# Performance work log

Measured on AMD Instinct MI355X. Metric: run time of the kernel, lower is better.

Reference implementation:

```python
import jax, jax.numpy as jnp
import numpy as np


def setup_inputs() -> dict:
    key = jax.random.key(0)
    embeddings = jax.random.normal(key, (4, 2048, 128), dtype=jnp.float32)
    return {"embeddings": embeddings}


def _pairwise_dist(x):
    # x: [N, D] -> Euclidean distance matrix [N, N] (matches torch.cdist, p=2)
    sq = jnp.sum(x * x, axis=-1)  # [N]
    d2 = sq[:, None] + sq[None, :] - 2.0 * (x @ x.T)
    d2 = jnp.maximum(d2, 0.0)
    # safe sqrt: exact 0 on the diagonal / coincident points, no NaN grads
    safe = jnp.where(d2 > 0.0, d2, 1.0)
    return jnp.where(d2 > 0.0, jnp.sqrt(safe), 0.0)


def reference(embeddings) -> jnp.ndarray:
    b, s, d = embeddings.shape
    x = embeddings.reshape(b * s, d)
    dist = _pairwise_dist(x)                 # [N, N]
    mean_dist = jnp.mean(dist)
    # torch.std default: unbiased (ddof=1) over all elements
    std_dist = jnp.std(dist, ddof=1)
    return std_dist / (mean_dist + 1e-08)
```

## Files before the change

kernel.cpp:

```cpp
#include <hip/hip_runtime.h>
#include <hip/hip_bf16.h>
#include <math.h>


#define NPTS   8192
#define DIM    128
#define BT     256
#define NT2    (NPTS / BT)
#define NBLK   (NT2 * (NT2 + 1) / 2)
#define NPREP  (NPTS / 32)
#define NTILES (NPTS / 128)
#define NTOTSQ (NTILES * NTILES)

typedef __attribute__((ext_vector_type(8))) short short8;
typedef __attribute__((ext_vector_type(4))) float f32x4;

typedef const __attribute__((address_space(1))) void* gas_ptr;
typedef __attribute__((address_space(3))) void* las_ptr;

__device__ __forceinline__ void gload16(const void* g, void* l) {
    __builtin_amdgcn_global_load_lds((gas_ptr)g, (las_ptr)l, 16, 0, 0);
}
__device__ __forceinline__ float fsqrt(float x) {
    return __builtin_amdgcn_sqrtf(x);
}

#define VMCNT(n) asm volatile("s_waitcnt vmcnt(" #n ")" ::: "memory")
#define RBAR()   __builtin_amdgcn_s_barrier()

__global__ __launch_bounds__(256)
void ph_prep(const float* __restrict__ x, ushort* __restrict__ xb,
             float* __restrict__ sq, float* __restrict__ cs_part)
{
    __shared__ float xs[32][129];
    const int tid = threadIdx.x;
    const int rw  = tid >> 3;
    const int row = blockIdx.x * 32 + rw;
    const int seg = tid & 7;
    const float4* p = reinterpret_cast<const float4*>(x + (size_t)row * DIM + seg * 16);
    float v[16];
    {
        float4 a = p[0], b = p[1], c = p[2], d = p[3];
        v[0]=a.x; v[1]=a.y; v[2]=a.z; v[3]=a.w;  v[4]=b.x; v[5]=b.y; v[6]=b.z; v[7]=b.w;
        v[8]=c.x; v[9]=c.y; v[10]=c.z; v[11]=c.w; v[12]=d.x; v[13]=d.y; v[14]=d.z; v[15]=d.w;
    }
    float s = 0.f;
    ushort h[16];
#pragma unroll
    for (int j = 0; j < 16; ++j) {
        __hip_bfloat16 hb = __float2bfloat16(v[j]);
        h[j] = *reinterpret_cast<ushort*>(&hb);
        s = fmaf(v[j], v[j], s);
        xs[rw][seg * 16 + j] = v[j];
    }
    short8 o0, o1;
#pragma unroll
    for (int j = 0; j < 8; ++j) { o0[j] = (short)h[j]; o1[j] = (short)h[j+8]; }
    short8* dst = reinterpret_cast<short8*>(xb + (size_t)row * DIM + seg * 16);
    dst[0] = o0; dst[1] = o1;
    s += __shfl_xor(s, 1); s += __shfl_xor(s, 2); s += __shfl_xor(s, 4);
    if (seg == 0) sq[row] = s;
    __syncthreads();
    if (tid < DIM) {
        float c = 0.f;
#pragma unroll 8
        for (int r = 0; r < 32; ++r) c += xs[r][tid];
        cs_part[blockIdx.x * DIM + tid] = c;
    }
}

__global__ __launch_bounds__(512)
void ph_gram(const ushort* __restrict__ xb, const float* __restrict__ sq,
             double* __restrict__ partials)
{
    const int f   = blockIdx.x;
    const int tid = threadIdx.x;

    int bi = (int)((65.0f - fsqrt((float)(4225 - 8 * f))) * 0.5f);
    while ((bi + 1) * 32 - ((bi + 1) * bi) / 2 <= f) ++bi;
    while (bi * 32 - (bi * (bi - 1)) / 2 > f) --bi;
    const int bj = bi + (f - (bi * 32 - (bi * (bi - 1)) / 2));

    __shared__ ushort Aq[4][BT * 32];
    __shared__ ushort Bq[4][BT * 32];
    __shared__ double rr[8];

    const int lane = tid & 63;
    const int wv   = tid >> 6;
    const int wr2  = wv >> 2;
    const int wc4  = wv & 3;

    const char* gA = (const char*)(xb + (size_t)bi * BT * DIM);
    const char* gB = (const char*)(xb + (size_t)bj * BT * DIM);

    const bool  stA  = wv < 4;
    const char* gsrc = stA ? gA : gB;
    const int   c0   = (wv & 3) * 4;
    const int   lrow = lane >> 2;
    const int   lks  = (lane & 3) * 16;

#define STAGE(q)                                                              \
    {                                                                         \
        char* dst_ = stA ? (char*)Aq[q] : (char*)Bq[q];                       \
        _Pragma("unroll")                                                     \
        for (int c = 0; c < 4; ++c) {                                         \
            const int chunk = c0 + c;                                         \
            const int row   = chunk * 16 + lrow;                              \
            const size_t go = (size_t)row * 256 + (q) * 64 + lks;             \
            gload16(gsrc + go, dst_ + chunk * 1024);                          \
        }                                                                     \
    }

    f32x4 acc[8][4];
#pragma unroll
    for (int m = 0; m < 8; ++m)
#pragma unroll
        for (int n = 0; n < 4; ++n) acc[m][n] = (f32x4){0.f, 0.f, 0.f, 0.f};

#define COMPUTE(q)                                                            \
    {                                                                         \
        const int kb = (lane >> 4) * 16;                                      \
        short8 af[8], bfr[4];                                                 \
        _Pragma("unroll")                                                     \
        for (int m = 0; m < 8; ++m) {                                         \
            const int row = wr2 * 128 + m * 16 + (lane & 15);                 \
            af[m] = *reinterpret_cast<const short8*>(                         \
                (const char*)Aq[q] + row * 64 + kb);                          \
        }                                                                     \
        _Pragma("unroll")                                                     \
        for (int n = 0; n < 4; ++n) {                                         \
            const int col = wc4 * 64 + n * 16 + (lane & 15);                  \
            bfr[n] = *reinterpret_cast<const short8*>(                        \
                (const char*)Bq[q] + col * 64 + kb);                          \
        }                                                                     \
        __builtin_amdgcn_s_setprio(1);                                        \
        _Pragma("unroll")                                                     \
        for (int m = 0; m < 8; ++m)                                           \
            _Pragma("unroll")                                                 \
            for (int n = 0; n < 4; ++n)                                       \
                acc[m][n] = __builtin_amdgcn_mfma_f32_16x16x32_bf16(          \
                    af[m], bfr[n], acc[m][n], 0, 0, 0);                       \
        __builtin_amdgcn_s_setprio(0);                                        \
    }

    STAGE(0);
    STAGE(1);
    VMCNT(4); RBAR();
    COMPUTE(0);
    STAGE(2);
    VMCNT(4); RBAR();
    COMPUTE(1);
    STAGE(3);

    const float* sqA = sq + bi * BT + wr2 * 128 + (lane >> 4) * 4;
    const float* sqB = sq + bj * BT + wc4 * 64 + (lane & 15);
    float4 na[4];
    float  nb[4];
#pragma unroll
    for (int m = 0; m < 4; ++m) na[m] = *reinterpret_cast<const float4*>(sqA + m * 32);
#pragma unroll
    for (int n = 0; n < 4; ++n) nb[n] = sqB[n * 16];

    VMCNT(12); RBAR();
    COMPUTE(2);
    VMCNT(8); RBAR();
    COMPUTE(3);
    VMCNT(0);

    float s1a = 0.f, s1b = 0.f, s1c = 0.f, s1d = 0.f;
    const bool diag = (bi == bj);
    if (!diag) {
#pragma unroll
        for (int m = 0; m < 4; ++m) {
            const float4 v = na[m];
#pragma unroll
            for (int n = 0; n < 4; ++n) {
                s1a += fsqrt(fmaxf(fmaf(-2.f, acc[2*m][n][0], v.x + nb[n]), 0.f));
                s1b += fsqrt(fmaxf(fmaf(-2.f, acc[2*m][n][1], v.y + nb[n]), 0.f));
                s1c += fsqrt(fmaxf(fmaf(-2.f, acc[2*m][n][2], v.z + nb[n]), 0.f));
                s1d += fsqrt(fmaxf(fmaf(-2.f, acc[2*m][n][3], v.w + nb[n]), 0.f));
            }
        }
    }
    if (!diag) {
#pragma unroll
        for (int m = 1; m < 8; m += 2) {
            const float4 v = *reinterpret_cast<const float4*>(sqA + m * 16);
#pragma unroll
            for (int n = 0; n < 4; ++n) {
                s1a += fsqrt(fmaxf(fmaf(-2.f, acc[m][n][0], v.x + nb[n]), 0.f));
                s1b += fsqrt(fmaxf(fmaf(-2.f, acc[m][n][1], v.y + nb[n]), 0.f));
                s1c += fsqrt(fmaxf(fmaf(-2.f, acc[m][n][2], v.z + nb[n]), 0.f));
                s1d += fsqrt(fmaxf(fmaf(-2.f, acc[m][n][3], v.w + nb[n]), 0.f));
            }
        }
    } else {
#pragma unroll
        for (int m = 0; m < 8; ++m) {
            const float4 v = *reinterpret_cast<const float4*>(sqA + m * 16);
            const float nav[4] = {v.x, v.y, v.z, v.w};
#pragma unroll
            for (int n = 0; n < 4; ++n) {
                const int col = wc4 * 64 + n * 16 + (lane & 15);
#pragma unroll
                for (int r = 0; r < 4; ++r) {
                    const int row = wr2 * 128 + m * 16 + (lane >> 4) * 4 + r;
                    float d = fmaxf(fmaf(-2.f, acc[m][n][r], nav[r] + nb[n]), 0.f);
                    if (row == col) d = 0.f;
                    s1a += fsqrt(d);
                }
            }
        }
    }
    float s1 = (s1a + s1b) + (s1c + s1d);
#pragma unroll
    for (int off = 1; off < 64; off <<= 1) s1 += __shfl_xor(s1, off);
    const double w = diag ? 1.0 : 2.0;
    if (lane == 0) rr[wv] = (double)s1 * w;
    __syncthreads();
    if (tid == 0) {
        double t1 = 0.0;
#pragma unroll
        for (int i = 0; i < 8; ++i) t1 += rr[i];
        partials[f] = t1;
    }
#undef STAGE
#undef COMPUTE
}

__global__ __launch_bounds__(256)
void ph_finalize(const double* __restrict__ partials, const float* __restrict__ sq,
                 const float* __restrict__ cs_part, float* __restrict__ out)
{
    __shared__ double r1[256], r2[256], r3[128];
    const int tid = threadIdx.x;
    double s1 = 0.0;
    for (int i = tid; i < NBLK; i += 256) s1 += partials[i];
    double sn = 0.0;
    for (int k = 0; k < NPTS / 256; ++k) sn += (double)sq[tid + k * 256];
    r1[tid] = s1; r2[tid] = sn;
    if (tid < DIM) {
        double c = 0.0;
        for (int b = 0; b < NPREP; ++b) c += (double)cs_part[b * DIM + tid];
        r3[tid] = c * c;
    }
    __syncthreads();
    for (int off = 128; off > 0; off >>= 1) {
        if (tid < off) {
            r1[tid] += r1[tid + off];
            r2[tid] += r2[tid + off];
            if (off >= 2 && tid < (off >> 1) && off <= 128) {}
        }
        __syncthreads();
    }
    for (int off = 64; off > 0; off >>= 1) {
        if (tid < off) r3[tid] += r3[tid + off];
        __syncthreads();
    }
    if (tid == 0) {
        const double M    = (double)NPTS * (double)NPTS;
        const double S1   = r1[0];
        const double S2   = 2.0 * (double)NPTS * r2[0] - 2.0 * r3[0];
        const double mean = S1 / M;
        double var = (S2 - S1 * S1 / M) / (M - 1.0);
        if (var < 0.0) var = 0.0;
        out[0] = (float)(sqrt(var) / (mean + 1e-8));
    }
}

#define LSTR 132
__global__ __launch_bounds__(256)
void ph_pair_kernel(const float* __restrict__ x, double* __restrict__ partials)
{
    const int bi  = blockIdx.y;
    const int bj  = blockIdx.x;
    const int tid = threadIdx.x;
    const int flat = bi * NTILES + bj;
    if (bj < bi) {
        if (tid == 0) { partials[2*flat] = 0.0; partials[2*flat+1] = 0.0; }
        return;
    }
    __shared__ __align__(16) float As[128 * LSTR];
    __shared__ __align__(16) float Bs[128 * LSTR];
    __shared__ float  nA[128];
    __shared__ float  nB[128];
    __shared__ double red1[256];
    __shared__ double red2[256];
    const float* Ab = x + (size_t)bi * 128 * DIM;
    const float* Bb = x + (size_t)bj * 128 * DIM;
#pragma unroll
    for (int it = 0; it < 16; ++it) {
        const int e   = (tid + it * 256) * 4;
        const int row = e >> 7;
        const int k   = e & 127;
        float4 va = *reinterpret_cast<const float4*>(Ab + e);
        As[(k+0)*LSTR + row] = va.x; As[(k+1)*LSTR + row] = va.y;
        As[(k+2)*LSTR + row] = va.z; As[(k+3)*LSTR + row] = va.w;
        float4 vb = *reinterpret_cast<const float4*>(Bb + e);
        Bs[(k+0)*LSTR + row] = vb.x; Bs[(k+1)*LSTR + row] = vb.y;
        Bs[(k+2)*LSTR + row] = vb.z; Bs[(k+3)*LSTR + row] = vb.w;
    }
    __syncthreads();
    if (tid < 128) {
        float s = 0.f;
#pragma unroll 8
        for (int k = 0; k < DIM; ++k) { float v = As[k*LSTR + tid]; s = fmaf(v, v, s); }
        nA[tid] = s;
    } else {
        const int r = tid - 128;
        float s = 0.f;
#pragma unroll 8
        for (int k = 0; k < DIM; ++k) { float v = Bs[k*LSTR + r]; s = fmaf(v, v, s); }
        nB[r] = s;
    }
    __syncthreads();
    const int tx = tid & 15, ty = tid >> 4;
    const int ra = ty * 8, cb = tx * 8;
    float acc[8][8];
#pragma unroll
    for (int r = 0; r < 8; ++r)
#pragma unroll
        for (int c = 0; c < 8; ++c) acc[r][c] = 0.f;
#pragma unroll 4
    for (int k = 0; k < DIM; ++k) {
        const float4 a0 = *reinterpret_cast<const float4*>(&As[k*LSTR + ra]);
        const float4 a1 = *reinterpret_cast<const float4*>(&As[k*LSTR + ra + 4]);
        const float4 b0 = *reinterpret_cast<const float4*>(&Bs[k*LSTR + cb]);
        const float4 b1 = *reinterpret_cast<const float4*>(&Bs[k*LSTR + cb + 4]);
        const float a[8] = {a0.x,a0.y,a0.z,a0.w,a1.x,a1.y,a1.z,a1.w};
        const float b[8] = {b0.x,b0.y,b0.z,b0.w,b1.x,b1.y,b1.z,b1.w};
#pragma unroll
        for (int r = 0; r < 8; ++r)
#pragma unroll
            for (int c = 0; c < 8; ++c)
                acc[r][c] = fmaf(a[r], b[c], acc[r][c]);
    }
    double s1 = 0.0, s2 = 0.0;
    const int gi0 = bi*128 + ra, gj0 = bj*128 + cb;
#pragma unroll
    for (int r = 0; r < 8; ++r) {
#pragma unroll
        for (int c = 0; c < 8; ++c) {
            float d2 = nA[ra+r] + nB[cb+c] - 2.0f * acc[r][c];
            d2 = fmaxf(d2, 0.0f);
            if (gi0 + r == gj0 + c) d2 = 0.0f;
            s1 += (double)sqrtf(d2);
            s2 += (double)d2;
        }
    }
    const double w = (bi == bj) ? 1.0 : 2.0;
    s1 *= w; s2 *= w;
    red1[tid] = s1; red2[tid] = s2;
    __syncthreads();
    for (int off = 128; off > 0; off >>= 1) {
        if (tid < off) { red1[tid] += red1[tid+off]; red2[tid] += red2[tid+off]; }
        __syncthreads();
    }
    if (tid == 0) { partials[2*flat] = red1[0]; partials[2*flat+1] = red2[0]; }
}

__global__ __launch_bounds__(256)
void ph_finalize_sq(const double* __restrict__ partials, float* __restrict__ out)
{
    __shared__ double r1[256], r2[256];
    const int tid = threadIdx.x;
    double s1 = 0.0, s2 = 0.0;
    for (int i = tid; i < NTOTSQ; i += 256) { s1 += partials[2*i]; s2 += partials[2*i+1]; }
    r1[tid] = s1; r2[tid] = s2;
    __syncthreads();
    for (int off = 128; off > 0; off >>= 1) {
        if (tid < off) { r1[tid] += r1[tid+off]; r2[tid] += r2[tid+off]; }
        __syncthreads();
    }
    if (tid == 0) {
        const double M    = (double)NPTS * (double)NPTS;
        const double mean = r1[0] / M;
        double var = (r2[0] - r1[0]*r1[0]/M) / (M - 1.0);
        if (var < 0.0) var = 0.0;
        out[0] = (float)(sqrt(var) / (mean + 1e-8));
    }
}

extern "C" void kernel_launch(void* const* d_in, const int* in_sizes, int n_in,
                              void* d_out, int out_size, void* d_ws, size_t ws_size,
                              hipStream_t stream)
{
    const float* x = (const float*)d_in[0];
    float* out     = (float*)d_out;

    const size_t XB_OFF = 0;
    const size_t SQ_OFF = (size_t)NPTS * DIM * sizeof(ushort);
    const size_t CS_OFF = SQ_OFF + NPTS * sizeof(float);
    const size_t PT_OFF = CS_OFF + (size_t)NPREP * DIM * sizeof(float);
    const size_t NEEDED = PT_OFF + (size_t)NBLK * sizeof(double);

    if (ws_size >= NEEDED) {
        ushort* xb       = (ushort*)((char*)d_ws + XB_OFF);
        float*  sq       = (float*) ((char*)d_ws + SQ_OFF);
        float*  cs_part  = (float*) ((char*)d_ws + CS_OFF);
        double* partials = (double*)((char*)d_ws + PT_OFF);

        ph_prep<<<NPREP, 256, 0, stream>>>(x, xb, sq, cs_part);
        ph_gram<<<NBLK, 512, 0, stream>>>(xb, sq, partials);
        ph_finalize<<<1, 256, 0, stream>>>(partials, sq, cs_part, out);
    } else {
        double* partials = (double*)d_ws;
        ph_pair_kernel<<<dim3(NTILES, NTILES), 256, 0, stream>>>(x, partials);
        ph_finalize_sq<<<1, 256, 0, stream>>>(partials, out);
    }
}
```

Before: 39.72 us.

## Split gram tile across 16 waves with XOR-swizzled LDS and two-stage K

The gram kernel now runs 1024 threads (16 waves), so each wave owns a 64x64 sub-tile instead of 128x64. K is staged in two halves of 64 into double LDS buffers with an XOR swizzle, replacing four 32-wide stages. The hand-placed vmcnt/barrier pipeline gives way to plain __syncthreads. The aim is more waves to hide latency, fewer LDS bank conflicts on fragment reads, and lower per-wave register pressure, at the cost of a shallower load/compute overlap.

```diff
diff --git a/kernel.cpp b/kernel.cpp
--- a/kernel.cpp
+++ b/kernel.cpp
@@ -24,9 +24,6 @@
 __device__ __forceinline__ float fsqrt(float x) {
     return __builtin_amdgcn_sqrtf(x);
 }
-
-#define VMCNT(n) asm volatile("s_waitcnt vmcnt(" #n ")" ::: "memory")
-#define RBAR()   __builtin_amdgcn_s_barrier()
 
 __global__ __launch_bounds__(256)
 void ph_prep(const float* __restrict__ x, ushort* __restrict__ xb,
@@ -69,7 +66,7 @@
     }
 }
 
-__global__ __launch_bounds__(512)
+__global__ __launch_bounds__(1024, 4)
 void ph_gram(const ushort* __restrict__ xb, const float* __restrict__ sq,
              double* __restrict__ partials)
 {
@@ -81,110 +78,90 @@
     while (bi * 32 - (bi * (bi - 1)) / 2 > f) --bi;
     const int bj = bi + (f - (bi * 32 - (bi * (bi - 1)) / 2));
 
-    __shared__ ushort Aq[4][BT * 32];
-    __shared__ ushort Bq[4][BT * 32];
-    __shared__ double rr[8];
+    __shared__ ushort A0[BT * 64], B0[BT * 64];
+    __shared__ ushort A1[BT * 64], B1[BT * 64];
+    __shared__ double rr[32];
 
     const int lane = tid & 63;
     const int wv   = tid >> 6;
-    const int wr2  = wv >> 2;
-    const int wc4  = wv & 3;
+    const int wr   = wv >> 2;
+    const int wc   = wv & 3;
 
     const char* gA = (const char*)(xb + (size_t)bi * BT * DIM);
     const char* gB = (const char*)(xb + (size_t)bj * BT * DIM);
 
-    const bool  stA  = wv < 4;
+    const bool  stA  = wv < 8;
     const char* gsrc = stA ? gA : gB;
-    const int   c0   = (wv & 3) * 4;
-    const int   lrow = lane >> 2;
-    const int   lks  = (lane & 3) * 16;
-
-#define STAGE(q)                                                              \
+    const int   c0   = (wv & 7) * 4;
+    const int   srow = lane >> 3;
+    const int   skb  = (lane & 7) * 16;
+
+#define STAGE(h, dA, dB)                                                      \
     {                                                                         \
-        char* dst_ = stA ? (char*)Aq[q] : (char*)Bq[q];                       \
+        char* dst_ = stA ? (char*)(dA) : (char*)(dB);                         \
         _Pragma("unroll")                                                     \
         for (int c = 0; c < 4; ++c) {                                         \
             const int chunk = c0 + c;                                         \
-            const int row   = chunk * 16 + lrow;                              \
-            const size_t go = (size_t)row * 256 + (q) * 64 + lks;             \
+            const int row   = chunk * 8 + srow;                               \
+            const size_t go = (size_t)row * 256 + (h) * 128                   \
+                              + (skb ^ ((row & 7) << 4));                     \
             gload16(gsrc + go, dst_ + chunk * 1024);                          \
         }                                                                     \
     }
 
-    f32x4 acc[8][4];
-#pragma unroll
-    for (int m = 0; m < 8; ++m)
+    f32x4 acc[4][4];
+#pragma unroll
+    for (int m = 0; m < 4; ++m)
 #pragma unroll
         for (int n = 0; n < 4; ++n) acc[m][n] = (f32x4){0.f, 0.f, 0.f, 0.f};
 
-#define COMPUTE(q)                                                            \
+#define COMPUTE(dA, dB)                                                       \
     {                                                                         \
-        const int kb = (lane >> 4) * 16;                                      \
-        short8 af[8], bfr[4];                                                 \
         _Pragma("unroll")                                                     \
-        for (int m = 0; m < 8; ++m) {                                         \
-            const int row = wr2 * 128 + m * 16 + (lane & 15);                 \
-            af[m] = *reinterpret_cast<const short8*>(                         \
-                (const char*)Aq[q] + row * 64 + kb);                          \
+        for (int ks = 0; ks < 2; ++ks) {                                      \
+            const int kb = ks * 64 + (lane >> 4) * 16;                        \
+            short8 af[4], bfr[4];                                             \
+            _Pragma("unroll")                                                 \
+            for (int m = 0; m < 4; ++m) {                                     \
+                const int row = wr * 64 + m * 16 + (lane & 15);               \
+                af[m] = *reinterpret_cast<const short8*>(                     \
+                    (const char*)(dA) + row * 128 + (kb ^ ((row & 7) << 4))); \
+            }                                                                 \
+            _Pragma("unroll")                                                 \
+            for (int n = 0; n < 4; ++n) {                                     \
+                const int col = wc * 64 + n * 16 + (lane & 15);               \
+                bfr[n] = *reinterpret_cast<const short8*>(                    \
+                    (const char*)(dB) + col * 128 + (kb ^ ((col & 7) << 4))); \
+            }                                                                 \
+            __builtin_amdgcn_s_setprio(1);                                    \
+            _Pragma("unroll")                                                 \
+            for (int m = 0; m < 4; ++m)                                       \
+                _Pragma("unroll")                                             \
+                for (int n = 0; n < 4; ++n)                                   \
+                    acc[m][n] = __builtin_amdgcn_mfma_f32_16x16x32_bf16(      \
+                        af[m], bfr[n], acc[m][n], 0, 0, 0);                   \
+            __builtin_amdgcn_s_setprio(0);                                    \
         }                                                                     \
-        _Pragma("unroll")                                                     \
-        for (int n = 0; n < 4; ++n) {                                         \
-            const int col = wc4 * 64 + n * 16 + (lane & 15);                  \
-            bfr[n] = *reinterpret_cast<const short8*>(                        \
-                (const char*)Bq[q] + col * 64 + kb);                          \
-        }                                                                     \
-        __builtin_amdgcn_s_setprio(1);                                        \
-        _Pragma("unroll")                                                     \
-        for (int m = 0; m < 8; ++m)                                           \
-            _Pragma("unroll")                                                 \
-            for (int n = 0; n < 4; ++n)                                       \
-                acc[m][n] = __builtin_amdgcn_mfma_f32_16x16x32_bf16(          \
-                    af[m], bfr[n], acc[m][n], 0, 0, 0);                       \
-        __builtin_amdgcn_s_setprio(0);                                        \
-    }
-
-    STAGE(0);
-    STAGE(1);
-    VMCNT(4); RBAR();
-    COMPUTE(0);
-    STAGE(2);
-    VMCNT(4); RBAR();
-    COMPUTE(1);
-    STAGE(3);
-
-    const float* sqA = sq + bi * BT + wr2 * 128 + (lane >> 4) * 4;
-    const float* sqB = sq + bj * BT + wc4 * 64 + (lane & 15);
-    float4 na[4];
-    float  nb[4];
-#pragma unroll
-    for (int m = 0; m < 4; ++m) na[m] = *reinterpret_cast<const float4*>(sqA + m * 32);
+    }
+
+    STAGE(0, A0, B0);
+    __syncthreads();
+    STAGE(1, A1, B1);
+    COMPUTE(A0, B0);
+    __syncthreads();
+    COMPUTE(A1, B1);
+
+    const float* sqA = sq + bi * BT + wr * 64 + (lane >> 4) * 4;
+    const float* sqB = sq + bj * BT + wc * 64 + (lane & 15);
+    float nb[4];
 #pragma unroll
     for (int n = 0; n < 4; ++n) nb[n] = sqB[n * 16];
-
-    VMCNT(12); RBAR();
-    COMPUTE(2);
-    VMCNT(8); RBAR();
-    COMPUTE(3);
-    VMCNT(0);
 
     float s1a = 0.f, s1b = 0.f, s1c = 0.f, s1d = 0.f;
     const bool diag = (bi == bj);
     if (!diag) {
 #pragma unroll
         for (int m = 0; m < 4; ++m) {
-            const float4 v = na[m];
-#pragma unroll
-            for (int n = 0; n < 4; ++n) {
-                s1a += fsqrt(fmaxf(fmaf(-2.f, acc[2*m][n][0], v.x + nb[n]), 0.f));
-                s1b += fsqrt(fmaxf(fmaf(-2.f, acc[2*m][n][1], v.y + nb[n]), 0.f));
-                s1c += fsqrt(fmaxf(fmaf(-2.f, acc[2*m][n][2], v.z + nb[n]), 0.f));
-                s1d += fsqrt(fmaxf(fmaf(-2.f, acc[2*m][n][3], v.w + nb[n]), 0.f));
-            }
-        }
-    }
-    if (!diag) {
-#pragma unroll
-        for (int m = 1; m < 8; m += 2) {
             const float4 v = *reinterpret_cast<const float4*>(sqA + m * 16);
 #pragma unroll
             for (int n = 0; n < 4; ++n) {
@@ -196,15 +173,15 @@
         }
     } else {
 #pragma unroll
-        for (int m = 0; m < 8; ++m) {
+        for (int m = 0; m < 4; ++m) {
             const float4 v = *reinterpret_cast<const float4*>(sqA + m * 16);
             const float nav[4] = {v.x, v.y, v.z, v.w};
 #pragma unroll
             for (int n = 0; n < 4; ++n) {
-                const int col = wc4 * 64 + n * 16 + (lane & 15);
+                const int col = wc * 64 + n * 16 + (lane & 15);
 #pragma unroll
                 for (int r = 0; r < 4; ++r) {
-                    const int row = wr2 * 128 + m * 16 + (lane >> 4) * 4 + r;
+                    const int row = wr * 64 + m * 16 + (lane >> 4) * 4 + r;
                     float d = fmaxf(fmaf(-2.f, acc[m][n][r], nav[r] + nb[n]), 0.f);
                     if (row == col) d = 0.f;
                     s1a += fsqrt(d);
@@ -221,7 +198,7 @@
     if (tid == 0) {
         double t1 = 0.0;
 #pragma unroll
-        for (int i = 0; i < 8; ++i) t1 += rr[i];
+        for (int i = 0; i < 16; ++i) t1 += rr[i];
         partials[f] = t1;
     }
 #undef STAGE
@@ -246,11 +223,7 @@
     }
     __syncthreads();
     for (int off = 128; off > 0; off >>= 1) {
-        if (tid < off) {
-            r1[tid] += r1[tid + off];
-            r2[tid] += r2[tid + off];
-            if (off >= 2 && tid < (off >> 1) && off <= 128) {}
-        }
+        if (tid < off) { r1[tid] += r1[tid + off]; r2[tid] += r2[tid + off]; }
         __syncthreads();
     }
     for (int off = 64; off > 0; off >>= 1) {
@@ -401,7 +374,7 @@
         double* partials = (double*)((char*)d_ws + PT_OFF);
 
         ph_prep<<<NPREP, 256, 0, stream>>>(x, xb, sq, cs_part);
-        ph_gram<<<NBLK, 512, 0, stream>>>(xb, sq, partials);
+        ph_gram<<<NBLK, 1024, 0, stream>>>(xb, sq, partials);
         ph_finalize<<<1, 256, 0, stream>>>(partials, sq, cs_part, out);
     } else {
         double* partials = (double*)d_ws;
```

Result: faster. 38.35 us (-3.4%).
